# Kernel optimization log

Hardware: AMD Instinct MI355X
Metric: run time of the kernel (lower is better)

## Reference

```python
import jax, jax.numpy as jnp
import numpy as np

EPS = 1e-12  # matches torch F.normalize default eps


def setup_inputs() -> dict:
    key = jax.random.key(0)
    k1, k2 = jax.random.split(key)
    n, c, h, w = 32, 512, 64, 64
    x1 = jax.random.normal(k1, (n, c, h, w), dtype=jnp.float32)
    x2 = jax.random.normal(k2, (n, c, h, w), dtype=jnp.float32)
    alpha = jnp.zeros((1,), dtype=jnp.float32)
    beta = jnp.zeros((1,), dtype=jnp.float32)
    return {"x1": x1, "x2": x2, "alpha": alpha, "beta": beta}


def reference(x1, x2, alpha, beta):
    n, c1, h, w = x1.shape
    c2 = x2.shape[1]
    hw = h * w
    x1_d = x1.reshape(n, c1, hw)
    x2_d = x2.reshape(n, c2, hw)
    # L2 normalize over spatial dim (dim=2), torch F.normalize semantics
    x1_f = x1_d / jnp.maximum(jnp.linalg.norm(x1_d, axis=2, keepdims=True), EPS)
    x2_f = x2_d / jnp.maximum(jnp.linalg.norm(x2_d, axis=2, keepdims=True), EPS)
    # [n, c1, c2] channel co-attention
    attention = jnp.einsum('nis,njs->nij', x1_f, x2_f)
    attn_x1 = jax.nn.softmax(attention, axis=2)              # softmax over c2
    fake_x1 = jnp.einsum('nij,njs->nis', attn_x1, x2_d).reshape(n, c1, h, w)
    attn_x2 = jax.nn.softmax(attention.transpose(0, 2, 1), axis=2)  # softmax over c1
    fake_x2 = jnp.einsum('nji,nis->njs', attn_x2, x1_d).reshape(n, c2, h, w)
    x1_out = alpha[0] * fake_x1 + x1
    x2_out = beta[0] * fake_x2 + x2
    return (x1_out, x2_out)
```

## Files before the change

### kernel.cpp

```cpp
#include <hip/hip_runtime.h>


#define N_B 32
#define C_  512
#define HW_ 4096

typedef float f32x4 __attribute__((ext_vector_type(4)));
typedef short s16x8 __attribute__((ext_vector_type(8)));

__device__ __forceinline__ unsigned pack_bf2(float lo, float hi) {
    unsigned a = __builtin_bit_cast(unsigned, lo);
    unsigned b = __builtin_bit_cast(unsigned, hi);
    return (a >> 16) | (b & 0xFFFF0000u);
}
__device__ __forceinline__ unsigned short f2bf(float f) {
    return (unsigned short)(__builtin_bit_cast(unsigned, f) >> 16);
}

__global__ void row_inv_norm(const float* __restrict__ x, float* __restrict__ invn) {
    const size_t row = blockIdx.x;
    const float* p = x + row * (size_t)HW_;
    const int t = threadIdx.x;
    float ss = 0.f;
#pragma unroll
    for (int jj = 0; jj < 4; ++jj) {
        float4 v = *(const float4*)(p + 4 * (t + 256 * jj));
        ss += v.x * v.x + v.y * v.y + v.z * v.z + v.w * v.w;
    }
    __shared__ float red[256];
    red[t] = ss;
    __syncthreads();
    for (int s = 128; s > 0; s >>= 1) {
        if (t < s) red[t] += red[t + s];
        __syncthreads();
    }
    if (t == 0) {
        float nrm = sqrtf(red[0]);
        invn[row] = 1.0f / fmaxf(nrm, 1e-12f);
    }
}

__global__ __launch_bounds__(256) void attn_gemm_mfma(
    const float* __restrict__ x1, const float* __restrict__ x2,
    const float* __restrict__ inv1, const float* __restrict__ inv2,
    float* __restrict__ att)
{
    const int n  = blockIdx.z;
    const int j0 = blockIdx.x * 128;
    const int m0 = blockIdx.y * 128;
    const float* Ag = x1 + (size_t)n * C_ * HW_;
    const float* Bg = x2 + (size_t)n * C_ * HW_;

    __shared__ char As[128 * 128];
    __shared__ char Bs[128 * 128];

    const int t    = threadIdx.x;
    const int lane = t & 63;
    const int w    = t >> 6;
    const int wr   = (w >> 1) * 64;
    const int wc   = (w & 1) * 64;
    const int fr   = lane & 15;
    const int fg   = lane >> 4;

    int srow[4], sslot[4], schunk[4];
#pragma unroll
    for (int p = 0; p < 4; ++p) {
        int idx   = p * 256 + t;
        srow[p]   = idx >> 3;
        sslot[p]  = idx & 7;
        schunk[p] = sslot[p] ^ (srow[p] & 7);
    }

    float a_st[4][8], b_st[4][8];
    f32x4 acc[4][4];
#pragma unroll
    for (int i = 0; i < 4; ++i)
#pragma unroll
        for (int j = 0; j < 4; ++j) acc[i][j] = (f32x4){0.f, 0.f, 0.f, 0.f};

    auto load_tiles = [&](int k0) {
#pragma unroll
        for (int p = 0; p < 4; ++p) {
            const float* ga = Ag + (size_t)(m0 + srow[p]) * HW_ + k0 + schunk[p] * 8;
            const float* gb = Bg + (size_t)(j0 + srow[p]) * HW_ + k0 + schunk[p] * 8;
            *(float4*)&a_st[p][0] = *(const float4*)ga;
            *(float4*)&a_st[p][4] = *(const float4*)(ga + 4);
            *(float4*)&b_st[p][0] = *(const float4*)gb;
            *(float4*)&b_st[p][4] = *(const float4*)(gb + 4);
        }
    };
    auto store_tiles = [&]() {
#pragma unroll
        for (int p = 0; p < 4; ++p) {
            uint4 pa, pb;
            pa.x = pack_bf2(a_st[p][0], a_st[p][1]);
            pa.y = pack_bf2(a_st[p][2], a_st[p][3]);
            pa.z = pack_bf2(a_st[p][4], a_st[p][5]);
            pa.w = pack_bf2(a_st[p][6], a_st[p][7]);
            pb.x = pack_bf2(b_st[p][0], b_st[p][1]);
            pb.y = pack_bf2(b_st[p][2], b_st[p][3]);
            pb.z = pack_bf2(b_st[p][4], b_st[p][5]);
            pb.w = pack_bf2(b_st[p][6], b_st[p][7]);
            const int off = srow[p] * 128 + sslot[p] * 16;
            *(uint4*)(As + off) = pa;
            *(uint4*)(Bs + off) = pb;
        }
    };
    auto compute = [&]() {
#pragma unroll
        for (int kk = 0; kk < 2; ++kk) {
            s16x8 af[4], bfv[4];
#pragma unroll
            for (int mi = 0; mi < 4; ++mi) {
                int row  = wr + mi * 16 + fr;
                int phys = (kk * 64 + fg * 16) ^ ((row & 7) << 4);
                af[mi] = __builtin_bit_cast(s16x8, *(const uint4*)(As + row * 128 + phys));
            }
#pragma unroll
            for (int ni = 0; ni < 4; ++ni) {
                int row  = wc + ni * 16 + fr;
                int phys = (kk * 64 + fg * 16) ^ ((row & 7) << 4);
                bfv[ni] = __builtin_bit_cast(s16x8, *(const uint4*)(Bs + row * 128 + phys));
            }
#pragma unroll
            for (int mi = 0; mi < 4; ++mi)
#pragma unroll
                for (int ni = 0; ni < 4; ++ni)
                    acc[mi][ni] = __builtin_amdgcn_mfma_f32_16x16x32_bf16(
                        af[mi], bfv[ni], acc[mi][ni], 0, 0, 0);
        }
    };

    load_tiles(0);
#pragma unroll 1
    for (int k0 = 0; k0 < HW_; k0 += 64) {
        __syncthreads();
        store_tiles();
        __syncthreads();
        if (k0 + 64 < HW_) load_tiles(k0 + 64);
        compute();
    }

    float s2v[4];
#pragma unroll
    for (int ni = 0; ni < 4; ++ni) s2v[ni] = inv2[n * C_ + j0 + wc + ni * 16 + fr];
#pragma unroll
    for (int mi = 0; mi < 4; ++mi)
#pragma unroll
        for (int r = 0; r < 4; ++r) {
            int m = m0 + wr + mi * 16 + fg * 4 + r;
            float s1 = inv1[n * C_ + m];
            float* orow = att + ((size_t)n * C_ + m) * C_ + j0 + wc;
#pragma unroll
            for (int ni = 0; ni < 4; ++ni)
                orow[ni * 16 + fr] = acc[mi][ni][r] * s1 * s2v[ni];
        }
}

__global__ void col_softmax_bf16(const float* __restrict__ att,
                                 unsigned short* __restrict__ attn2b) {
    const int n  = blockIdx.y;
    const int j0 = blockIdx.x * 64;
    const int t  = threadIdx.x;
    const int col = j0 + (t & 63);
    const int sl  = t >> 6;
    const float* base = att + (size_t)n * C_ * C_;

    float m = -INFINITY, l = 0.f;
    for (int i = sl * 128; i < sl * 128 + 128; ++i) {
        float v = base[(size_t)i * C_ + col];
        float mn = fmaxf(m, v);
        l = l * __expf(m - mn) + __expf(v - mn);
        m = mn;
    }
    __shared__ float ms[4][64], ls[4][64];
    ms[sl][t & 63] = m;
    ls[sl][t & 63] = l;
    __syncthreads();
    float M = fmaxf(fmaxf(ms[0][t & 63], ms[1][t & 63]),
                    fmaxf(ms[2][t & 63], ms[3][t & 63]));
    float L = 0.f;
#pragma unroll
    for (int s = 0; s < 4; ++s) L += ls[s][t & 63] * __expf(ms[s][t & 63] - M);
    const float inv = 1.0f / L;
    unsigned short* outp = attn2b + ((size_t)n * C_ + col) * C_;
    for (int i = sl * 128; i < sl * 128 + 128; ++i)
        outp[i] = f2bf(__expf(base[(size_t)i * C_ + col] - M) * inv);
}

__global__ void row_softmax_bf16(float* __restrict__ att) {
    const size_t row = blockIdx.x;
    float* p = att + row * (size_t)C_;
    const int t = threadIdx.x;
    float2 v = *(const float2*)(p + 2 * t);
    __shared__ float red[256];
    red[t] = fmaxf(v.x, v.y);
    __syncthreads();
    for (int s = 128; s > 0; s >>= 1) {
        if (t < s) red[t] = fmaxf(red[t], red[t + s]);
        __syncthreads();
    }
    const float M = red[0];
    __syncthreads();
    float e0 = __expf(v.x - M), e1 = __expf(v.y - M);
    red[t] = e0 + e1;
    __syncthreads();
    for (int s = 128; s > 0; s >>= 1) {
        if (t < s) red[t] += red[t + s];
        __syncthreads();
    }
    const float inv = 1.0f / red[0];
    ((unsigned*)p)[t] = pack_bf2(e0 * inv, e1 * inv);
}

__global__ __launch_bounds__(256) void gemm_epi_mfma(
    const unsigned short* __restrict__ Aall, const int pitchA,
    const float* __restrict__ Ball, const float* __restrict__ Xall,
    const float* __restrict__ scal, float* __restrict__ outAll)
{
    const int n  = blockIdx.z;
    const int s0 = blockIdx.x * 128;
    const int m0 = blockIdx.y * 128;
    const unsigned short* Ag = Aall + (size_t)n * C_ * pitchA;
    const float* Bg = Ball + (size_t)n * C_ * HW_;
    const float* Xg = Xall + (size_t)n * C_ * HW_;
    float* out = outAll + (size_t)n * C_ * HW_;

    __shared__ char As[128 * 128];
    __shared__ char Bs[128 * 144];

    const int t    = threadIdx.x;
    const int lane = t & 63;
    const int w    = t >> 6;
    const int wr   = (w >> 1) * 64;
    const int wc   = (w & 1) * 64;
    const int fr   = lane & 15;
    const int fg   = lane >> 4;

    uint4 a_st[4];
    float b_st[8][4];
    f32x4 acc[4][4];
#pragma unroll
    for (int i = 0; i < 4; ++i)
#pragma unroll
        for (int j = 0; j < 4; ++j) acc[i][j] = (f32x4){0.f, 0.f, 0.f, 0.f};

    auto load_a = [&](int k0) {
#pragma unroll
        for (int p = 0; p < 4; ++p) {
            int idx = p * 256 + t;
            int r   = idx >> 3;
            int c   = (idx & 7) ^ (r & 7);
            a_st[p] = *(const uint4*)(Ag + (size_t)(m0 + r) * pitchA + k0 + c * 8);
        }
    };
    auto store_a = [&]() {
#pragma unroll
        for (int p = 0; p < 4; ++p) {
            int idx = p * 256 + t;
            *(uint4*)(As + idx * 16) = a_st[p];
        }
    };
    auto load_b = [&](int k0) {
#pragma unroll
        for (int p = 0; p < 8; ++p) {
            int idx = p * 256 + t;
            int s   = idx & 127;
            int k4  = (idx >> 7) * 4;
            const float* g = Bg + (size_t)(k0 + k4) * HW_ + s0 + s;
#pragma unroll
            for (int e = 0; e < 4; ++e) b_st[p][e] = g[(size_t)e * HW_];
        }
    };
    auto store_b = [&]() {
#pragma unroll
        for (int p = 0; p < 8; ++p) {
            int idx = p * 256 + t;
            int s   = idx & 127;
            int k4  = (idx >> 7) * 4;
            uint2 pk;
            pk.x = pack_bf2(b_st[p][0], b_st[p][1]);
            pk.y = pack_bf2(b_st[p][2], b_st[p][3]);
            *(uint2*)(Bs + s * 144 + k4 * 2) = pk;
        }
    };
    auto compute = [&]() {
#pragma unroll
        for (int kk = 0; kk < 2; ++kk) {
            s16x8 af[4], bfv[4];
#pragma unroll
            for (int mi = 0; mi < 4; ++mi) {
                int row  = wr + mi * 16 + fr;
                int phys = (kk * 64 + fg * 16) ^ ((row & 7) << 4);
                af[mi] = __builtin_bit_cast(s16x8, *(const uint4*)(As + row * 128 + phys));
            }
#pragma unroll
            for (int ni = 0; ni < 4; ++ni) {
                int col = wc + ni * 16 + fr;
                bfv[ni] = __builtin_bit_cast(s16x8,
                    *(const uint4*)(Bs + col * 144 + kk * 64 + fg * 16));
            }
#pragma unroll
            for (int mi = 0; mi < 4; ++mi)
#pragma unroll
                for (int ni = 0; ni < 4; ++ni)
                    acc[mi][ni] = __builtin_amdgcn_mfma_f32_16x16x32_bf16(
                        af[mi], bfv[ni], acc[mi][ni], 0, 0, 0);
        }
    };

    load_a(0);
    load_b(0);
#pragma unroll 1
    for (int ks = 0; ks < 8; ++ks) {
        __syncthreads();
        store_a();
        store_b();
        __syncthreads();
        if (ks < 7) { load_a((ks + 1) * 64); load_b((ks + 1) * 64); }
        compute();
    }

    const float sc = scal[0];
#pragma unroll
    for (int mi = 0; mi < 4; ++mi)
#pragma unroll
        for (int r = 0; r < 4; ++r) {
            int m = m0 + wr + mi * 16 + fg * 4 + r;
            const float* xrow = Xg + (size_t)m * HW_ + s0 + wc;
            float*       orow = out + (size_t)m * HW_ + s0 + wc;
#pragma unroll
            for (int ni = 0; ni < 4; ++ni)
                orow[ni * 16 + fr] = fmaf(sc, acc[mi][ni][r], xrow[ni * 16 + fr]);
        }
}

extern "C" void kernel_launch(void* const* d_in, const int* in_sizes, int n_in,
                              void* d_out, int out_size, void* d_ws, size_t ws_size,
                              hipStream_t stream) {
    const float* x1    = (const float*)d_in[0];
    const float* x2    = (const float*)d_in[1];
    const float* alpha = (const float*)d_in[2];
    const float* beta  = (const float*)d_in[3];
    float* out = (float*)d_out;

    float* inv1 = (float*)d_ws;
    float* inv2 = inv1 + (size_t)N_B * C_;
    float* att  = inv2 + (size_t)N_B * C_;
    unsigned short* attn1b = (unsigned short*)att;
    unsigned short* attn2b = (unsigned short*)d_out;
    float* out1 = out;
    float* out2 = out + (size_t)N_B * C_ * HW_;

    row_inv_norm<<<N_B * C_, 256, 0, stream>>>(x1, inv1);
    row_inv_norm<<<N_B * C_, 256, 0, stream>>>(x2, inv2);

    attn_gemm_mfma<<<dim3(4, 4, N_B), 256, 0, stream>>>(x1, x2, inv1, inv2, att);

    col_softmax_bf16<<<dim3(8, N_B), 256, 0, stream>>>(att, attn2b);
    row_softmax_bf16<<<N_B * C_, 256, 0, stream>>>(att);

    gemm_epi_mfma<<<dim3(HW_ / 128, C_ / 128, N_B), 256, 0, stream>>>(
        attn2b, C_, x1, x2, beta, out2);
    gemm_epi_mfma<<<dim3(HW_ / 128, C_ / 128, N_B), 256, 0, stream>>>(
        attn1b, 2 * C_, x2, x1, alpha, out1);
}
```

Measured before the change: 1.649 ms.

## Precompute bf16 copies and transposes of inputs with fused norm pass

New measurement: 2.221 ms. 34.7% more time.

```diff
diff --git a/kernel.cpp b/kernel.cpp
--- a/kernel.cpp
+++ b/kernel.cpp
@@ -17,61 +17,79 @@
     return (unsigned short)(__builtin_bit_cast(unsigned, f) >> 16);
 }
 
-__global__ void row_inv_norm(const float* __restrict__ x, float* __restrict__ invn) {
-    const size_t row = blockIdx.x;
-    const float* p = x + row * (size_t)HW_;
-    const int t = threadIdx.x;
-    float ss = 0.f;
-#pragma unroll
-    for (int jj = 0; jj < 4; ++jj) {
-        float4 v = *(const float4*)(p + 4 * (t + 256 * jj));
-        ss += v.x * v.x + v.y * v.y + v.z * v.z + v.w * v.w;
-    }
-    __shared__ float red[256];
-    red[t] = ss;
-    __syncthreads();
-    for (int s = 128; s > 0; s >>= 1) {
-        if (t < s) red[t] += red[t + s];
-        __syncthreads();
-    }
-    if (t == 0) {
-        float nrm = sqrtf(red[0]);
-        invn[row] = 1.0f / fmaxf(nrm, 1e-12f);
+__global__ void zero_f32(float* __restrict__ p, int n) {
+    int i = blockIdx.x * 256 + threadIdx.x;
+    if (i < n) p[i] = 0.f;
+}
+
+__global__ __launch_bounds__(256) void prep(const float* __restrict__ x,
+    unsigned short* __restrict__ xb, unsigned short* __restrict__ xbt,
+    float* __restrict__ nrm)
+{
+    const int n = blockIdx.z, c0 = blockIdx.y * 64, s0 = blockIdx.x * 256;
+    const int t = threadIdx.x, lane = t & 63, w = t >> 6;
+    __shared__ unsigned short tp[64][258];
+    const float* src = x + ((size_t)n * C_ + c0) * (size_t)HW_ + s0;
+
+#pragma unroll
+    for (int i = 0; i < 16; ++i) {
+        const int row = i * 4 + w;
+        float4 v = *(const float4*)(src + (size_t)row * HW_ + lane * 4);
+        float ss = v.x * v.x + v.y * v.y + v.z * v.z + v.w * v.w;
+#pragma unroll
+        for (int d = 1; d < 64; d <<= 1) ss += __shfl_xor(ss, d, 64);
+        if (lane == 0) atomicAdd(&nrm[n * C_ + c0 + row], ss);
+        unsigned lo = pack_bf2(v.x, v.y), hi = pack_bf2(v.z, v.w);
+        unsigned short* xrow = xb + ((size_t)n * C_ + c0 + row) * (size_t)HW_ + s0 + lane * 4;
+        uint2 u; u.x = lo; u.y = hi;
+        *(uint2*)xrow = u;
+        unsigned* tl = (unsigned*)&tp[row][lane * 4];
+        tl[0] = lo; tl[1] = hi;
+    }
+    __syncthreads();
+    unsigned pk[32];
+#pragma unroll
+    for (int c = 0; c < 64; c += 2)
+        pk[c >> 1] = (unsigned)tp[c][t] | ((unsigned)tp[c + 1][t] << 16);
+    unsigned short* orow = xbt + ((size_t)n * HW_ + s0 + t) * (size_t)C_ + c0;
+#pragma unroll
+    for (int q = 0; q < 8; ++q) {
+        uint4 u;
+        u.x = pk[q * 4 + 0]; u.y = pk[q * 4 + 1];
+        u.z = pk[q * 4 + 2]; u.w = pk[q * 4 + 3];
+        *(uint4*)(orow + q * 8) = u;
     }
 }
 
 __global__ __launch_bounds__(256) void attn_gemm_mfma(
-    const float* __restrict__ x1, const float* __restrict__ x2,
-    const float* __restrict__ inv1, const float* __restrict__ inv2,
+    const unsigned short* __restrict__ x1b, const unsigned short* __restrict__ x2b,
+    const float* __restrict__ nrm1, const float* __restrict__ nrm2,
     float* __restrict__ att)
 {
-    const int n  = blockIdx.z;
-    const int j0 = blockIdx.x * 128;
-    const int m0 = blockIdx.y * 128;
-    const float* Ag = x1 + (size_t)n * C_ * HW_;
-    const float* Bg = x2 + (size_t)n * C_ * HW_;
-
-    __shared__ char As[128 * 128];
-    __shared__ char Bs[128 * 128];
-
-    const int t    = threadIdx.x;
-    const int lane = t & 63;
-    const int w    = t >> 6;
-    const int wr   = (w >> 1) * 64;
-    const int wc   = (w & 1) * 64;
-    const int fr   = lane & 15;
-    const int fg   = lane >> 4;
-
-    int srow[4], sslot[4], schunk[4];
+    const int flat = blockIdx.x + 4 * (blockIdx.y + 4 * blockIdx.z);
+    const int id   = (flat & 7) * 64 + (flat >> 3);
+    const int j0 = (id & 3) * 128, m0 = ((id >> 2) & 3) * 128, n = id >> 4;
+    const unsigned short* Ag = x1b + (size_t)n * C_ * HW_;
+    const unsigned short* Bg = x2b + (size_t)n * C_ * HW_;
+
+    __shared__ __align__(16) char As[128 * 128];
+    __shared__ __align__(16) char Bs[128 * 128];
+
+    const int t = threadIdx.x, lane = t & 63, w = t >> 6;
+    const int wr = (w >> 1) * 64, wc = (w & 1) * 64;
+    const int fr = lane & 15, fg = lane >> 4;
+
+    int srow[4], soff[4], sgoff[4];
 #pragma unroll
     for (int p = 0; p < 4; ++p) {
-        int idx   = p * 256 + t;
-        srow[p]   = idx >> 3;
-        sslot[p]  = idx & 7;
-        schunk[p] = sslot[p] ^ (srow[p] & 7);
-    }
-
-    float a_st[4][8], b_st[4][8];
+        int idx = p * 256 + t;
+        int r = idx >> 3, sl = idx & 7;
+        srow[p]  = r;
+        soff[p]  = r * 128 + sl * 16;
+        sgoff[p] = (sl ^ (r & 7)) * 8;
+    }
+
+    uint4 a_st[4], b_st[4];
     f32x4 acc[4][4];
 #pragma unroll
     for (int i = 0; i < 4; ++i)
@@ -81,29 +99,15 @@
     auto load_tiles = [&](int k0) {
 #pragma unroll
         for (int p = 0; p < 4; ++p) {
-            const float* ga = Ag + (size_t)(m0 + srow[p]) * HW_ + k0 + schunk[p] * 8;
-            const float* gb = Bg + (size_t)(j0 + srow[p]) * HW_ + k0 + schunk[p] * 8;
-            *(float4*)&a_st[p][0] = *(const float4*)ga;
-            *(float4*)&a_st[p][4] = *(const float4*)(ga + 4);
-            *(float4*)&b_st[p][0] = *(const float4*)gb;
-            *(float4*)&b_st[p][4] = *(const float4*)(gb + 4);
+            a_st[p] = *(const uint4*)(Ag + (size_t)(m0 + srow[p]) * HW_ + k0 + sgoff[p]);
+            b_st[p] = *(const uint4*)(Bg + (size_t)(j0 + srow[p]) * HW_ + k0 + sgoff[p]);
         }
     };
     auto store_tiles = [&]() {
 #pragma unroll
         for (int p = 0; p < 4; ++p) {
-            uint4 pa, pb;
-            pa.x = pack_bf2(a_st[p][0], a_st[p][1]);
-            pa.y = pack_bf2(a_st[p][2], a_st[p][3]);
-            pa.z = pack_bf2(a_st[p][4], a_st[p][5]);
-            pa.w = pack_bf2(a_st[p][6], a_st[p][7]);
-            pb.x = pack_bf2(b_st[p][0], b_st[p][1]);
-            pb.y = pack_bf2(b_st[p][2], b_st[p][3]);
-            pb.z = pack_bf2(b_st[p][4], b_st[p][5]);
-            pb.w = pack_bf2(b_st[p][6], b_st[p][7]);
-            const int off = srow[p] * 128 + sslot[p] * 16;
-            *(uint4*)(As + off) = pa;
-            *(uint4*)(Bs + off) = pb;
+            *(uint4*)(As + soff[p]) = a_st[p];
+            *(uint4*)(Bs + soff[p]) = b_st[p];
         }
     };
     auto compute = [&]() {
@@ -141,19 +145,23 @@
         compute();
     }
 
-    float s2v[4];
-#pragma unroll
-    for (int ni = 0; ni < 4; ++ni) s2v[ni] = inv2[n * C_ + j0 + wc + ni * 16 + fr];
+    float i2[4];
+#pragma unroll
+    for (int ni = 0; ni < 4; ++ni) {
+        float ss = nrm2[n * C_ + j0 + wc + ni * 16 + fr];
+        i2[ni] = 1.0f / fmaxf(sqrtf(ss), 1e-12f);
+    }
 #pragma unroll
     for (int mi = 0; mi < 4; ++mi)
 #pragma unroll
         for (int r = 0; r < 4; ++r) {
             int m = m0 + wr + mi * 16 + fg * 4 + r;
-            float s1 = inv1[n * C_ + m];
+            float ss1 = nrm1[n * C_ + m];
+            float i1 = 1.0f / fmaxf(sqrtf(ss1), 1e-12f);
             float* orow = att + ((size_t)n * C_ + m) * C_ + j0 + wc;
 #pragma unroll
             for (int ni = 0; ni < 4; ++ni)
-                orow[ni * 16 + fr] = acc[mi][ni][r] * s1 * s2v[ni];
+                orow[ni * 16 + fr] = acc[mi][ni][r] * i1 * i2[ni];
         }
 }
 
@@ -167,6 +175,7 @@
     const float* base = att + (size_t)n * C_ * C_;
 
     float m = -INFINITY, l = 0.f;
+#pragma unroll 4
     for (int i = sl * 128; i < sl * 128 + 128; ++i) {
         float v = base[(size_t)i * C_ + col];
         float mn = fmaxf(m, v);
@@ -184,6 +193,7 @@
     for (int s = 0; s < 4; ++s) L += ls[s][t & 63] * __expf(ms[s][t & 63] - M);
     const float inv = 1.0f / L;
     unsigned short* outp = attn2b + ((size_t)n * C_ + col) * C_;
+#pragma unroll 4
     for (int i = sl * 128; i < sl * 128 + 128; ++i)
         outp[i] = f2bf(__expf(base[(size_t)i * C_ + col] - M) * inv);
 }
@@ -215,73 +225,54 @@
 
 __global__ __launch_bounds__(256) void gemm_epi_mfma(
     const unsigned short* __restrict__ Aall, const int pitchA,
-    const float* __restrict__ Ball, const float* __restrict__ Xall,
-    const float* __restrict__ scal, float* __restrict__ outAll)
+    const unsigned short* __restrict__ Bt,
+    const float* __restrict__ Xall, const float* __restrict__ scal,
+    float* __restrict__ outAll)
 {
-    const int n  = blockIdx.z;
-    const int s0 = blockIdx.x * 128;
-    const int m0 = blockIdx.y * 128;
+    const int flat = blockIdx.x + 32 * (blockIdx.y + 4 * blockIdx.z);
+    const int id   = (flat & 7) * 512 + (flat >> 3);
+    const int s0 = (id & 31) * 128, m0 = ((id >> 5) & 3) * 128, n = id >> 7;
     const unsigned short* Ag = Aall + (size_t)n * C_ * pitchA;
-    const float* Bg = Ball + (size_t)n * C_ * HW_;
+    const unsigned short* Bg = Bt   + (size_t)n * HW_ * C_;
     const float* Xg = Xall + (size_t)n * C_ * HW_;
     float* out = outAll + (size_t)n * C_ * HW_;
 
-    __shared__ char As[128 * 128];
-    __shared__ char Bs[128 * 144];
-
-    const int t    = threadIdx.x;
-    const int lane = t & 63;
-    const int w    = t >> 6;
-    const int wr   = (w >> 1) * 64;
-    const int wc   = (w & 1) * 64;
-    const int fr   = lane & 15;
-    const int fg   = lane >> 4;
-
-    uint4 a_st[4];
-    float b_st[8][4];
+    __shared__ __align__(16) char As[128 * 128];
+    __shared__ __align__(16) char Bs[128 * 128];
+
+    const int t = threadIdx.x, lane = t & 63, w = t >> 6;
+    const int wr = (w >> 1) * 64, wc = (w & 1) * 64;
+    const int fr = lane & 15, fg = lane >> 4;
+
+    int srow[4], soff[4], sgoff[4];
+#pragma unroll
+    for (int p = 0; p < 4; ++p) {
+        int idx = p * 256 + t;
+        int r = idx >> 3, sl = idx & 7;
+        srow[p]  = r;
+        soff[p]  = r * 128 + sl * 16;
+        sgoff[p] = (sl ^ (r & 7)) * 8;
+    }
+
+    uint4 a_st[4], b_st[4];
     f32x4 acc[4][4];
 #pragma unroll
     for (int i = 0; i < 4; ++i)
 #pragma unroll
         for (int j = 0; j < 4; ++j) acc[i][j] = (f32x4){0.f, 0.f, 0.f, 0.f};
 
-    auto load_a = [&](int k0) {
+    auto load_tiles = [&](int k0) {
 #pragma unroll
         for (int p = 0; p < 4; ++p) {
-            int idx = p * 256 + t;
-            int r   = idx >> 3;
-            int c   = (idx & 7) ^ (r & 7);
-            a_st[p] = *(const uint4*)(Ag + (size_t)(m0 + r) * pitchA + k0 + c * 8);
-        }
-    };
-    auto store_a = [&]() {
+            a_st[p] = *(const uint4*)(Ag + (size_t)(m0 + srow[p]) * pitchA + k0 + sgoff[p]);
+            b_st[p] = *(const uint4*)(Bg + (size_t)(s0 + srow[p]) * C_ + k0 + sgoff[p]);
+        }
+    };
+    auto store_tiles = [&]() {
 #pragma unroll
         for (int p = 0; p < 4; ++p) {
-            int idx = p * 256 + t;
-            *(uint4*)(As + idx * 16) = a_st[p];
-        }
-    };
-    auto load_b = [&](int k0) {
-#pragma unroll
-        for (int p = 0; p < 8; ++p) {
-            int idx = p * 256 + t;
-            int s   = idx & 127;
-            int k4  = (idx >> 7) * 4;
-            const float* g = Bg + (size_t)(k0 + k4) * HW_ + s0 + s;
-#pragma unroll
-            for (int e = 0; e < 4; ++e) b_st[p][e] = g[(size_t)e * HW_];
-        }
-    };
-    auto store_b = [&]() {
-#pragma unroll
-        for (int p = 0; p < 8; ++p) {
-            int idx = p * 256 + t;
-            int s   = idx & 127;
-            int k4  = (idx >> 7) * 4;
-            uint2 pk;
-            pk.x = pack_bf2(b_st[p][0], b_st[p][1]);
-            pk.y = pack_bf2(b_st[p][2], b_st[p][3]);
-            *(uint2*)(Bs + s * 144 + k4 * 2) = pk;
+            *(uint4*)(As + soff[p]) = a_st[p];
+            *(uint4*)(Bs + soff[p]) = b_st[p];
         }
     };
     auto compute = [&]() {
@@ -296,9 +287,9 @@
             }
 #pragma unroll
             for (int ni = 0; ni < 4; ++ni) {
-                int col = wc + ni * 16 + fr;
-                bfv[ni] = __builtin_bit_cast(s16x8,
-                    *(const uint4*)(Bs + col * 144 + kk * 64 + fg * 16));
+                int row  = wc + ni * 16 + fr;
+                int phys = (kk * 64 + fg * 16) ^ ((row & 7) << 4);
+                bfv[ni] = __builtin_bit_cast(s16x8, *(const uint4*)(Bs + row * 128 + phys));
             }
 #pragma unroll
             for (int mi = 0; mi < 4; ++mi)
@@ -309,15 +300,13 @@
         }
     };
 
-    load_a(0);
-    load_b(0);
+    load_tiles(0);
 #pragma unroll 1
     for (int ks = 0; ks < 8; ++ks) {
         __syncthreads();
-        store_a();
-        store_b();
-        __syncthreads();
-        if (ks < 7) { load_a((ks + 1) * 64); load_b((ks + 1) * 64); }
+        store_tiles();
+        __syncthreads();
+        if (ks < 7) load_tiles((ks + 1) * 64);
         compute();
     }
 
@@ -344,24 +333,27 @@
     const float* beta  = (const float*)d_in[3];
     float* out = (float*)d_out;
 
-    float* inv1 = (float*)d_ws;
-    float* inv2 = inv1 + (size_t)N_B * C_;
-    float* att  = inv2 + (size_t)N_B * C_;
+    float* nrm1 = (float*)d_ws;
+    float* nrm2 = nrm1 + (size_t)N_B * C_;
+    float* att  = nrm2 + (size_t)N_B * C_;
+    unsigned short* attn2b = (unsigned short*)(att + (size_t)N_B * C_ * C_);
+    unsigned short* x1b  = attn2b + (size_t)N_B * C_ * C_;
+    unsigned short* x2b  = x1b  + (size_t)N_B * C_ * HW_;
+    unsigned short* x1bt = x2b  + (size_t)N_B * C_ * HW_;
+    unsigned short* x2bt = x1bt + (size_t)N_B * C_ * HW_;
     unsigned short* attn1b = (unsigned short*)att;
-    unsigned short* attn2b = (unsigned short*)d_out;
     float* out1 = out;
     float* out2 = out + (size_t)N_B * C_ * HW_;
 
-    row_inv_norm<<<N_B * C_, 256, 0, stream>>>(x1, inv1);
-    row_inv_norm<<<N_B * C_, 256, 0, stream>>>(x2, inv2);
-
-    attn_gemm_mfma<<<dim3(4, 4, N_B), 256, 0, stream>>>(x1, x2, inv1, inv2, att);
+    zero_f32<<<(2 * N_B * C_ + 255) / 256, 256, 0, stream>>>(nrm1, 2 * N_B * C_);
+    prep<<<dim3(16, 8, N_B), 256, 0, stream>>>(x1, x1b, x1bt, nrm1);
+    prep<<<dim3(16, 8, N_B), 256, 0, stream>>>(x2, x2b, x2bt, nrm2);
+
+    attn_gemm_mfma<<<dim3(4, 4, N_B), 256, 0, stream>>>(x1b, x2b, nrm1, nrm2, att);
 
     col_softmax_bf16<<<dim3(8, N_B), 256, 0, stream>>>(att, attn2b);
     row_softmax_bf16<<<N_B * C_, 256, 0, stream>>>(att);
 
-    gemm_epi_mfma<<<dim3(HW_ / 128, C_ / 128, N_B), 256, 0, stream>>>(
-        attn2b, C_, x1, x2, beta, out2);
-    gemm_epi_mfma<<<dim3(HW_ / 128, C_ / 128, N_B), 256, 0, stream>>>(
-        attn1b, 2 * C_, x2, x1, alpha, out1);
-}
+    gemm_epi_mfma<<<dim3(32, 4, N_B), 256, 0, stream>>>(attn2b, C_, x1bt, x2, beta, out2);
+    gemm_epi_mfma<<<dim3(32, 4, N_B), 256, 0, stream>>>(attn1b, 2 * C_, x2bt, x1, alpha, out1);
+}
```
